# Performance work log

Hardware: AMD Instinct MI355X
Metric: run time of the kernel (lower is better)

Reference implementation:

```python
import jax, jax.numpy as jnp
import numpy as np
from jax import lax

N = 100000      # nodes
F_IN = 128      # dataset.num_features
H = 64          # hidden
E = 1600000     # edges
G = 1000        # graphs (equal-sized, contiguous)
PER = N // G    # nodes per graph = 100
K = 30          # sort-pool k
KS = 3          # conv1d kernel = num_layers


def setup_inputs() -> dict:
    key = jax.random.key(0)
    ks = jax.random.split(key, 20)
    lin = lambda k, i, o: (jax.random.normal(k, (i, o), jnp.float32) / np.sqrt(i)).astype(jnp.float32)
    return {
        "x": jax.random.normal(ks[0], (N, F_IN), jnp.float32),
        "src": jax.random.randint(ks[1], (E,), 0, N, dtype=jnp.int32),
        "dst": jax.random.randint(ks[2], (E,), 0, N, dtype=jnp.int32),
        "num_graphs": G,
        # SAGEConv 1: lin_l (aggr, with bias), lin_r (self, no bias)
        "wl1": lin(ks[3], F_IN, H), "wr1": lin(ks[4], F_IN, H), "b1": jnp.zeros((H,), jnp.float32),
        "wl2": lin(ks[5], H, H), "wr2": lin(ks[6], H, H), "b2": jnp.zeros((H,), jnp.float32),
        "wl3": lin(ks[7], H, H), "wr3": lin(ks[8], H, H), "b3": jnp.zeros((H,), jnp.float32),
        # Conv1d(hidden=64 -> 32, kernel=3): weight [O, I, K]
        "cw": (jax.random.normal(ks[9], (32, H, KS), jnp.float32) / np.sqrt(H * KS)).astype(jnp.float32),
        "cb": jnp.zeros((32,), jnp.float32),
        "w1": lin(ks[10], 32 * (K - KS + 1), H), "bb1": jnp.zeros((H,), jnp.float32),
        "w2": lin(ks[11], H, 1), "bb2": jnp.zeros((1,), jnp.float32),
    }


def _sage(x, src, dst, wl, wr, b, n):
    # PyG SAGEConv (mean aggr): lin_l(mean_{j->i} x_j) + lin_r(x_i)
    msum = jax.ops.segment_sum(x[src], dst, num_segments=n)           # [N, F]
    cnt = jax.ops.segment_sum(jnp.ones((src.shape[0],), x.dtype), dst, num_segments=n)
    mean = msum / jnp.maximum(cnt, 1.0)[:, None]
    return mean @ wl + b + x @ wr


def reference(x, src, dst, num_graphs, wl1, wr1, b1, wl2, wr2, b2, wl3, wr3, b3, cw, cb, w1, bb1, w2, bb2):
    n = x.shape[0]
    h = jax.nn.relu(_sage(x, src, dst, wl1, wr1, b1, n))
    h = jax.nn.relu(_sage(h, src, dst, wl2, wr2, b2, n))
    h = jax.nn.relu(_sage(h, src, dst, wl3, wr3, b3, n))
    # SortAggregation(k): per-graph, sort nodes by last feature channel (desc), keep top-k.
    # batch = contiguous equal-sized graphs -> dense reshape is exact.
    hg = h.reshape(num_graphs, PER, H)                                # [G, PER, H]
    order = jnp.argsort(-hg[:, :, -1], axis=1)[:, :K]                 # [G, K]
    topk = jnp.take_along_axis(hg, order[:, :, None], axis=1)         # [G, K, H]
    xc = jnp.transpose(topk, (0, 2, 1))                               # [G, H, K]
    y = lax.conv_general_dilated(xc, cw, (1,), 'VALID',
                                 dimension_numbers=('NCH', 'OIH', 'NCH'))
    y = jax.nn.relu(y + cb[None, :, None])                            # [G, 32, K-KS+1]
    y = y.reshape(num_graphs, -1)
    y = jax.nn.relu(y @ w1 + bb1)
    # dropout: eval mode -> identity
    return y @ w2 + bb2                                               # [G, 1]
```

## Files before the change

### kernel.cpp

```cpp
#include <hip/hip_runtime.h>

#define NN 100000
#define EE 1600000
#define GG 1000
#define PERG 100
#define KK 30
#define HH 64

#define NB 782
#define CAP 4096
#define CHB 4096
#define BUCKET_BLOCKS ((EE + CHB - 1) / CHB)
#define PROJ_BLOCKS ((NN + 127) / 128)

__global__ __launch_bounds__(1024) void zero_int(int* p, int n) {
  int i = blockIdx.x * 1024 + threadIdx.x;
  if (i < n) p[i] = 0;
}

__device__ __forceinline__ void bucket_body(int bid, float* smem,
                                            const int* __restrict__ src,
                                            const int* __restrict__ dst,
                                            int* __restrict__ gcur,
                                            int* __restrict__ pairs) {
  int* lhist = (int*)smem;
  int* lbase = lhist + NB;
  int* lcur = lbase + NB;
  const int t = threadIdx.x;
  const int c0 = bid * CHB;
  const int c1 = min(c0 + CHB, EE);
  for (int b = t; b < NB; b += 256) {
    lhist[b] = 0;
    lcur[b] = 0;
  }
  __syncthreads();
  for (int e = c0 + t; e < c1; e += 256) atomicAdd(&lhist[dst[e] >> 7], 1);
  __syncthreads();
  for (int b = t; b < NB; b += 256) {
    int c = lhist[b];
    lbase[b] = c ? atomicAdd(&gcur[b], c) : 0;
  }
  __syncthreads();
  for (int e = c0 + t; e < c1; e += 256) {
    int d = dst[e];
    int b = d >> 7;
    int p = atomicAdd(&lcur[b], 1);
    pairs[b * CAP + lbase[b] + p] = (src[e] << 7) | (d & 127);
  }
}

template <int K>
__device__ __forceinline__ void proj_body(int bid, float* smem,
                                          const float* __restrict__ X,
                                          const float* __restrict__ WL,
                                          const float* __restrict__ WR,
                                          float* __restrict__ P,
                                          float* __restrict__ R) {
  constexpr int BM = 128, BK = 32, XSP = 40, WSP = 144;
  float* xs = smem;
  float* ws = smem + BM * XSP;
  const int t = threadIdx.x;
  const int row0 = bid * BM;
  const int tc = t & 15, tr = t >> 4;
  const int wcol = tc * 8 + (tc >> 2) * 4;

  float acc[8][8];
#pragma unroll
  for (int i = 0; i < 8; ++i)
#pragma unroll
    for (int j = 0; j < 8; ++j) acc[i][j] = 0.f;

  for (int k0 = 0; k0 < K; k0 += BK) {
    __syncthreads();
    for (int idx = t; idx < BM * 8; idx += 256) {
      int r = idx >> 3, c = idx & 7;
      int row = row0 + r;
      float4 v = make_float4(0.f, 0.f, 0.f, 0.f);
      if (row < NN) v = *reinterpret_cast<const float4*>(&X[(size_t)row * K + k0 + c * 4]);
      *reinterpret_cast<float4*>(&xs[r * XSP + c * 4]) = v;
    }
    for (int idx = t; idx < BK * 16; idx += 256) {
      int kr = idx >> 4, c4 = idx & 15;
      int gcl = c4 >> 1;
      int off = gcl * 8 + (gcl >> 2) * 4 + (c4 & 1) * 4;
      *reinterpret_cast<float4*>(&ws[kr * WSP + off]) =
          *reinterpret_cast<const float4*>(&WL[(k0 + kr) * 64 + c4 * 4]);
      int g2 = gcl + 8;
      int off2 = g2 * 8 + (g2 >> 2) * 4 + (c4 & 1) * 4;
      *reinterpret_cast<float4*>(&ws[kr * WSP + off2]) =
          *reinterpret_cast<const float4*>(&WR[(k0 + kr) * 64 + c4 * 4]);
    }
    __syncthreads();
    for (int kk4 = 0; kk4 < BK; kk4 += 4) {
      float4 a[8];
#pragma unroll
      for (int i = 0; i < 8; ++i)
        a[i] = *reinterpret_cast<const float4*>(&xs[(tr + 16 * i) * XSP + kk4]);
#pragma unroll
      for (int kk = 0; kk < 4; ++kk) {
        float4 b0 = *reinterpret_cast<const float4*>(&ws[(kk4 + kk) * WSP + wcol]);
        float4 b1 = *reinterpret_cast<const float4*>(&ws[(kk4 + kk) * WSP + wcol + 4]);
        float bv[8] = {b0.x, b0.y, b0.z, b0.w, b1.x, b1.y, b1.z, b1.w};
#pragma unroll
        for (int i = 0; i < 8; ++i) {
          float av = (kk == 0) ? a[i].x : (kk == 1) ? a[i].y : (kk == 2) ? a[i].z : a[i].w;
#pragma unroll
          for (int j = 0; j < 8; ++j) acc[i][j] = fmaf(av, bv[j], acc[i][j]);
        }
      }
    }
  }

  float* OUT = (tc < 8) ? P : R;
  int cb = (tc & 7) * 8;
#pragma unroll
  for (int i = 0; i < 8; ++i) {
    int row = row0 + tr + 16 * i;
    if (row < NN) {
      *reinterpret_cast<float4*>(&OUT[(size_t)row * 64 + cb]) =
          make_float4(acc[i][0], acc[i][1], acc[i][2], acc[i][3]);
      *reinterpret_cast<float4*>(&OUT[(size_t)row * 64 + cb + 4]) =
          make_float4(acc[i][4], acc[i][5], acc[i][6], acc[i][7]);
    }
  }
}

__global__ __launch_bounds__(256) void fused_bucket_proj(const int* __restrict__ src,
                                                         const int* __restrict__ dst,
                                                         int* __restrict__ gcur,
                                                         int* __restrict__ pairs,
                                                         const float* __restrict__ X,
                                                         const float* __restrict__ WL,
                                                         const float* __restrict__ WR,
                                                         float* __restrict__ P,
                                                         float* __restrict__ R) {
  __shared__ float smem[128 * 40 + 32 * 144];
  if (blockIdx.x < BUCKET_BLOCKS)
    bucket_body(blockIdx.x, smem, src, dst, gcur, pairs);
  else
    proj_body<128>(blockIdx.x - BUCKET_BLOCKS, smem, X, WL, WR, P, R);
}

template <int K>
__global__ __launch_bounds__(256) void proj_kernel(const float* __restrict__ X,
                                                   const float* __restrict__ WL,
                                                   const float* __restrict__ WR,
                                                   float* __restrict__ P,
                                                   float* __restrict__ R) {
  __shared__ float smem[128 * 40 + 32 * 144];
  proj_body<K>(blockIdx.x, smem, X, WL, WR, P, R);
}

__global__ __launch_bounds__(256) void csr_kernel(const int* __restrict__ gcur,
                                                  const int* __restrict__ pairs,
                                                  int* __restrict__ row_start,
                                                  int* __restrict__ cnt,
                                                  int* __restrict__ eidx) {
  __shared__ int vals[CAP];
  __shared__ int hist[128];
  __shared__ int offs[128];
  __shared__ int cur[128];
  __shared__ int red[4];
  const int b = blockIdx.x;
  const int t = threadIdx.x;
  int s = 0;
  for (int i = t; i < b; i += 256) s += gcur[i];
#pragma unroll
  for (int off = 32; off > 0; off >>= 1) s += __shfl_xor(s, off);
  if ((t & 63) == 0) red[t >> 6] = s;
  if (t < 128) {
    hist[t] = 0;
    cur[t] = 0;
  }
  __syncthreads();
  const int base = red[0] + red[1] + red[2] + red[3];
  const int nb = gcur[b];
  for (int i = t; i < nb; i += 256) {
    int v = pairs[b * CAP + i];
    vals[i] = v;
    atomicAdd(&hist[v & 127], 1);
  }
  __syncthreads();
  if (t < 128) {
    int ss = 0;
    for (int m = 0; m < t; ++m) ss += hist[m];
    offs[t] = ss;
    int node = b * 128 + t;
    if (node < NN) {
      row_start[node] = base + ss;
      cnt[node] = hist[t];
    }
  }
  __syncthreads();
  for (int i = t; i < nb; i += 256) {
    int v = vals[i];
    int ld = v & 127;
    int p = atomicAdd(&cur[ld], 1);
    eidx[base + offs[ld] + p] = v >> 7;
  }
}

__global__ __launch_bounds__(256) void agg_kernel(const float* __restrict__ P,
                                                  const float* __restrict__ R,
                                                  const float* __restrict__ bias,
                                                  const int* __restrict__ row_start,
                                                  const int* __restrict__ cnt,
                                                  const int* __restrict__ eidx,
                                                  float* __restrict__ h,
                                                  float* __restrict__ keys) {
  int wid = (blockIdx.x * 256 + threadIdx.x) >> 6;
  int lane = threadIdx.x & 63;
  if (wid >= NN) return;
  const int q = lane >> 4;
  const int ql = lane & 15;
  const int base = row_start[wid];
  const int deg = cnt[wid];
  float4 a0 = make_float4(0.f, 0.f, 0.f, 0.f);
  float4 a1 = make_float4(0.f, 0.f, 0.f, 0.f);

  for (int e0 = 0; e0 < deg; e0 += 64) {
    const int m = min(64, deg - e0);
    int idx = (lane < m) ? eidx[base + e0 + lane] : 0;
    for (int j = 0; j < m; j += 16) {
      const int eA = j + q, eB = j + 4 + q, eC = j + 8 + q, eD = j + 12 + q;
      const int sA = __shfl(idx, min(eA, m - 1));
      const int sB = __shfl(idx, min(eB, m - 1));
      const int sC = __shfl(idx, min(eC, m - 1));
      const int sD = __shfl(idx, min(eD, m - 1));
      const float wA = (eA < m) ? 1.f : 0.f;
      const float wB = (eB < m) ? 1.f : 0.f;
      const float wC = (eC < m) ? 1.f : 0.f;
      const float wD = (eD < m) ? 1.f : 0.f;
      float4 vA = *reinterpret_cast<const float4*>(&P[(size_t)sA * 64 + ql * 4]);
      float4 vB = *reinterpret_cast<const float4*>(&P[(size_t)sB * 64 + ql * 4]);
      float4 vC = *reinterpret_cast<const float4*>(&P[(size_t)sC * 64 + ql * 4]);
      float4 vD = *reinterpret_cast<const float4*>(&P[(size_t)sD * 64 + ql * 4]);
      a0.x = fmaf(wA, vA.x, a0.x); a0.y = fmaf(wA, vA.y, a0.y);
      a0.z = fmaf(wA, vA.z, a0.z); a0.w = fmaf(wA, vA.w, a0.w);
      a1.x = fmaf(wB, vB.x, a1.x); a1.y = fmaf(wB, vB.y, a1.y);
      a1.z = fmaf(wB, vB.z, a1.z); a1.w = fmaf(wB, vB.w, a1.w);
      a0.x = fmaf(wC, vC.x, a0.x); a0.y = fmaf(wC, vC.y, a0.y);
      a0.z = fmaf(wC, vC.z, a0.z); a0.w = fmaf(wC, vC.w, a0.w);
      a1.x = fmaf(wD, vD.x, a1.x); a1.y = fmaf(wD, vD.y, a1.y);
      a1.z = fmaf(wD, vD.z, a1.z); a1.w = fmaf(wD, vD.w, a1.w);
    }
  }

  float4 acc = make_float4(a0.x + a1.x, a0.y + a1.y, a0.z + a1.z, a0.w + a1.w);
#pragma unroll
  for (int d = 16; d < 64; d <<= 1) {
    acc.x += __shfl_xor(acc.x, d);
    acc.y += __shfl_xor(acc.y, d);
    acc.z += __shfl_xor(acc.z, d);
    acc.w += __shfl_xor(acc.w, d);
  }

  if (q == 0) {
    const float dv = fmaxf((float)deg, 1.0f);
    float4 r4 = *reinterpret_cast<const float4*>(&R[(size_t)wid * 64 + ql * 4]);
    float4 b4 = *reinterpret_cast<const float4*>(&bias[ql * 4]);
    float4 o;
    o.x = fmaxf(acc.x / dv + b4.x + r4.x, 0.f);
    o.y = fmaxf(acc.y / dv + b4.y + r4.y, 0.f);
    o.z = fmaxf(acc.z / dv + b4.z + r4.z, 0.f);
    o.w = fmaxf(acc.w / dv + b4.w + r4.w, 0.f);
    *reinterpret_cast<float4*>(&h[(size_t)wid * 64 + ql * 4]) = o;
    if (keys != nullptr && ql == 15) keys[wid] = o.w;
  }
}

__global__ __launch_bounds__(256) void head_kernel(const float* __restrict__ h,
                                                   const float* __restrict__ keysArr,
                                                   const float* __restrict__ cw,
                                                   const float* __restrict__ cb,
                                                   const float* __restrict__ w1,
                                                   const float* __restrict__ bb1,
                                                   const float* __restrict__ w2,
                                                   const float* __restrict__ bb2,
                                                   float* __restrict__ out) {
  __shared__ float key[PERG];
  __shared__ int sel[KK];
  __shared__ float feat[34 * 65];
  __shared__ float cwT[192 * 33];
  __shared__ float z[896];
  __shared__ float psum[256];
  const int g = blockIdx.x;
  const int t = threadIdx.x;

  for (int idx = t; idx < 32 * 192; idx += 256) {
    int o = idx / 192, k = idx % 192;
    cwT[k * 33 + o] = cw[idx];
  }
  if (t < PERG) key[t] = keysArr[g * PERG + t];
  __syncthreads();

  if (t < PERG) {
    float kv = key[t];
    int r = 0;
    for (int m = 0; m < PERG; ++m) {
      float km = key[m];
      r += (int)((km > kv) || (km == kv && m < t));
    }
    if (r < KK) sel[r] = t;
  }
  __syncthreads();

  for (int idx = t; idx < KK * HH; idx += 256) {
    int r = idx >> 6, f = idx & 63;
    feat[r * 65 + f] = h[(size_t)(g * PERG + sel[r]) * HH + f];
  }
  __syncthreads();

  {
    const int o = t & 31;
    const int pg = t >> 5;
    float zacc[4] = {0.f, 0.f, 0.f, 0.f};
    int i = 0, tt = 0;
    for (int k = 0; k < 192; ++k) {
      float c = cwT[k * 33 + o];
#pragma unroll
      for (int j = 0; j < 4; ++j) {
        int p = pg + 8 * j;
        zacc[j] = fmaf(c, feat[(p + tt) * 65 + i], zacc[j]);
      }
      if (++tt == 3) {
        tt = 0;
        ++i;
      }
    }
    float cbo = cb[o];
#pragma unroll
    for (int j = 0; j < 4; ++j) {
      int p = pg + 8 * j;
      if (p < 28) z[o * 28 + p] = fmaxf(zacc[j] + cbo, 0.f);
    }
  }
  __syncthreads();

  {
    const int hh = t & 63;
    const int quarter = t >> 6;
    const int q0 = quarter * 224;
    float acc = 0.f;
    for (int q = 0; q < 224; ++q)
      acc = fmaf(z[q0 + q], w1[(size_t)(q0 + q) * 64 + hh], acc);
    psum[t] = acc;
  }
  __syncthreads();

  if (t < 64) {
    float o1 = fmaxf(bb1[t] + psum[t] + psum[t + 64] + psum[t + 128] + psum[t + 192], 0.f);
    float v = o1 * w2[t];
#pragma unroll
    for (int off = 32; off > 0; off >>= 1) v += __shfl_down(v, off);
    if (t == 0) out[g] = v + bb2[0];
  }
}

extern "C" void kernel_launch(void* const* d_in, const int* in_sizes, int n_in,
                              void* d_out, int out_size, void* d_ws, size_t ws_size,
                              hipStream_t stream) {
  const float* x = (const float*)d_in[0];
  const int* src = (const int*)d_in[1];
  const int* dst = (const int*)d_in[2];
  const float* wl1 = (const float*)d_in[4];
  const float* wr1 = (const float*)d_in[5];
  const float* b1 = (const float*)d_in[6];
  const float* wl2 = (const float*)d_in[7];
  const float* wr2 = (const float*)d_in[8];
  const float* b2 = (const float*)d_in[9];
  const float* wl3 = (const float*)d_in[10];
  const float* wr3 = (const float*)d_in[11];
  const float* b3 = (const float*)d_in[12];
  const float* cw = (const float*)d_in[13];
  const float* cb = (const float*)d_in[14];
  const float* w1 = (const float*)d_in[15];
  const float* bb1 = (const float*)d_in[16];
  const float* w2 = (const float*)d_in[17];
  const float* bb2 = (const float*)d_in[18];
  float* out = (float*)d_out;

  char* w = (char*)d_ws;
  auto carve = [&](size_t bytes) {
    char* p = w;
    w += (bytes + 255) & ~(size_t)255;
    return p;
  };
  int* row_start = (int*)carve((size_t)NN * 4);
  int* cnt = (int*)carve((size_t)NN * 4);
  int* eidx = (int*)carve((size_t)EE * 4);
  float* P = (float*)carve((size_t)NN * 64 * 4);
  float* R = (float*)carve((size_t)NN * 64 * 4);
  float* hbuf = (float*)carve((size_t)NN * 64 * 4);
  float* keys = (float*)carve((size_t)NN * 4);
  int* gcur = (int*)carve((size_t)NB * 4);
  int* pairs = (int*)hbuf;

  zero_int<<<1, 1024, 0, stream>>>(gcur, NB);
  fused_bucket_proj<<<BUCKET_BLOCKS + PROJ_BLOCKS, 256, 0, stream>>>(
      src, dst, gcur, pairs, x, wl1, wr1, P, R);
  csr_kernel<<<NB, 256, 0, stream>>>(gcur, pairs, row_start, cnt, eidx);

  const int aggGrid = (NN + 3) / 4;
  agg_kernel<<<aggGrid, 256, 0, stream>>>(P, R, b1, row_start, cnt, eidx, hbuf, nullptr);
  proj_kernel<64><<<PROJ_BLOCKS, 256, 0, stream>>>(hbuf, wl2, wr2, P, R);
  agg_kernel<<<aggGrid, 256, 0, stream>>>(P, R, b2, row_start, cnt, eidx, hbuf, nullptr);
  proj_kernel<64><<<PROJ_BLOCKS, 256, 0, stream>>>(hbuf, wl3, wr3, P, R);
  agg_kernel<<<aggGrid, 256, 0, stream>>>(P, R, b3, row_start, cnt, eidx, hbuf, keys);
  head_kernel<<<GG, 256, 0, stream>>>(hbuf, keys, cw, cb, w1, bb1, w2, bb2, out);
}
```

Baseline: 482.1 us.

## Replace shared-memory tiled projection GEMM with one-row-per-thread register GEMM

```diff
diff --git a/kernel.cpp b/kernel.cpp
--- a/kernel.cpp
+++ b/kernel.cpp
@@ -11,21 +11,21 @@
 #define CAP 4096
 #define CHB 4096
 #define BUCKET_BLOCKS ((EE + CHB - 1) / CHB)
-#define PROJ_BLOCKS ((NN + 127) / 128)
+#define RGB ((NN + 255) / 256)
 
 __global__ __launch_bounds__(1024) void zero_int(int* p, int n) {
   int i = blockIdx.x * 1024 + threadIdx.x;
   if (i < n) p[i] = 0;
 }
 
-__device__ __forceinline__ void bucket_body(int bid, float* smem,
+__device__ __forceinline__ void bucket_body(int bid,
                                             const int* __restrict__ src,
                                             const int* __restrict__ dst,
                                             int* __restrict__ gcur,
                                             int* __restrict__ pairs) {
-  int* lhist = (int*)smem;
-  int* lbase = lhist + NB;
-  int* lcur = lbase + NB;
+  __shared__ int lhist[NB];
+  __shared__ int lbase[NB];
+  __shared__ int lcur[NB];
   const int t = threadIdx.x;
   const int c0 = bid * CHB;
   const int c1 = min(c0 + CHB, EE);
@@ -50,77 +50,46 @@
 }
 
 template <int K>
-__device__ __forceinline__ void proj_body(int bid, float* smem,
-                                          const float* __restrict__ X,
-                                          const float* __restrict__ WL,
-                                          const float* __restrict__ WR,
-                                          float* __restrict__ P,
-                                          float* __restrict__ R) {
-  constexpr int BM = 128, BK = 32, XSP = 40, WSP = 144;
-  float* xs = smem;
-  float* ws = smem + BM * XSP;
-  const int t = threadIdx.x;
-  const int row0 = bid * BM;
-  const int tc = t & 15, tr = t >> 4;
-  const int wcol = tc * 8 + (tc >> 2) * 4;
-
-  float acc[8][8];
-#pragma unroll
-  for (int i = 0; i < 8; ++i)
-#pragma unroll
-    for (int j = 0; j < 8; ++j) acc[i][j] = 0.f;
-
-  for (int k0 = 0; k0 < K; k0 += BK) {
-    __syncthreads();
-    for (int idx = t; idx < BM * 8; idx += 256) {
-      int r = idx >> 3, c = idx & 7;
-      int row = row0 + r;
-      float4 v = make_float4(0.f, 0.f, 0.f, 0.f);
-      if (row < NN) v = *reinterpret_cast<const float4*>(&X[(size_t)row * K + k0 + c * 4]);
-      *reinterpret_cast<float4*>(&xs[r * XSP + c * 4]) = v;
-    }
-    for (int idx = t; idx < BK * 16; idx += 256) {
-      int kr = idx >> 4, c4 = idx & 15;
-      int gcl = c4 >> 1;
-      int off = gcl * 8 + (gcl >> 2) * 4 + (c4 & 1) * 4;
-      *reinterpret_cast<float4*>(&ws[kr * WSP + off]) =
-          *reinterpret_cast<const float4*>(&WL[(k0 + kr) * 64 + c4 * 4]);
-      int g2 = gcl + 8;
-      int off2 = g2 * 8 + (g2 >> 2) * 4 + (c4 & 1) * 4;
-      *reinterpret_cast<float4*>(&ws[kr * WSP + off2]) =
-          *reinterpret_cast<const float4*>(&WR[(k0 + kr) * 64 + c4 * 4]);
-    }
-    __syncthreads();
-    for (int kk4 = 0; kk4 < BK; kk4 += 4) {
-      float4 a[8];
-#pragma unroll
-      for (int i = 0; i < 8; ++i)
-        a[i] = *reinterpret_cast<const float4*>(&xs[(tr + 16 * i) * XSP + kk4]);
-#pragma unroll
-      for (int kk = 0; kk < 4; ++kk) {
-        float4 b0 = *reinterpret_cast<const float4*>(&ws[(kk4 + kk) * WSP + wcol]);
-        float4 b1 = *reinterpret_cast<const float4*>(&ws[(kk4 + kk) * WSP + wcol + 4]);
-        float bv[8] = {b0.x, b0.y, b0.z, b0.w, b1.x, b1.y, b1.z, b1.w};
-#pragma unroll
-        for (int i = 0; i < 8; ++i) {
-          float av = (kk == 0) ? a[i].x : (kk == 1) ? a[i].y : (kk == 2) ? a[i].z : a[i].w;
-#pragma unroll
-          for (int j = 0; j < 8; ++j) acc[i][j] = fmaf(av, bv[j], acc[i][j]);
-        }
-      }
-    }
-  }
-
-  float* OUT = (tc < 8) ? P : R;
-  int cb = (tc & 7) * 8;
-#pragma unroll
-  for (int i = 0; i < 8; ++i) {
-    int row = row0 + tr + 16 * i;
+__device__ __forceinline__ void proj_rowgemm(int row,
+                                             const float* __restrict__ X,
+                                             const float* __restrict__ WL,
+                                             const float* __restrict__ WR,
+                                             float* __restrict__ P,
+                                             float* __restrict__ R) {
+  float xr[K];
+  if (row < NN) {
+#pragma unroll
+    for (int kq = 0; kq < K / 4; ++kq) {
+      float4 v = *reinterpret_cast<const float4*>(&X[(size_t)row * K + kq * 4]);
+      xr[kq * 4 + 0] = v.x;
+      xr[kq * 4 + 1] = v.y;
+      xr[kq * 4 + 2] = v.z;
+      xr[kq * 4 + 3] = v.w;
+    }
+  } else {
+#pragma unroll
+    for (int k = 0; k < K; ++k) xr[k] = 0.f;
+  }
+
+#pragma unroll 1
+  for (int c = 0; c < 8; ++c) {
+    const float* __restrict__ W = (c < 4) ? (WL + c * 16) : (WR + (c - 4) * 16);
+    float acc[16];
+#pragma unroll
+    for (int j = 0; j < 16; ++j) acc[j] = 0.f;
+#pragma unroll
+    for (int k = 0; k < K; ++k) {
+      const float* __restrict__ wk = W + (size_t)k * 64;
+#pragma unroll
+      for (int j = 0; j < 16; ++j) acc[j] = fmaf(xr[k], wk[j], acc[j]);
+    }
     if (row < NN) {
-      *reinterpret_cast<float4*>(&OUT[(size_t)row * 64 + cb]) =
-          make_float4(acc[i][0], acc[i][1], acc[i][2], acc[i][3]);
-      *reinterpret_cast<float4*>(&OUT[(size_t)row * 64 + cb + 4]) =
-          make_float4(acc[i][4], acc[i][5], acc[i][6], acc[i][7]);
+      float* __restrict__ OUT = (c < 4) ? P : R;
+      const size_t o = (size_t)row * 64 + (c & 3) * 16;
+#pragma unroll
+      for (int j4 = 0; j4 < 4; ++j4)
+        *reinterpret_cast<float4*>(&OUT[o + j4 * 4]) =
+            make_float4(acc[j4 * 4], acc[j4 * 4 + 1], acc[j4 * 4 + 2], acc[j4 * 4 + 3]);
     }
   }
 }
@@ -134,11 +103,12 @@
                                                          const float* __restrict__ WR,
                                                          float* __restrict__ P,
                                                          float* __restrict__ R) {
-  __shared__ float smem[128 * 40 + 32 * 144];
-  if (blockIdx.x < BUCKET_BLOCKS)
-    bucket_body(blockIdx.x, smem, src, dst, gcur, pairs);
-  else
-    proj_body<128>(blockIdx.x - BUCKET_BLOCKS, smem, X, WL, WR, P, R);
+  if (blockIdx.x < BUCKET_BLOCKS) {
+    bucket_body(blockIdx.x, src, dst, gcur, pairs);
+  } else {
+    int row = (blockIdx.x - BUCKET_BLOCKS) * 256 + threadIdx.x;
+    proj_rowgemm<128>(row, X, WL, WR, P, R);
+  }
 }
 
 template <int K>
@@ -147,8 +117,8 @@
                                                    const float* __restrict__ WR,
                                                    float* __restrict__ P,
                                                    float* __restrict__ R) {
-  __shared__ float smem[128 * 40 + 32 * 144];
-  proj_body<K>(blockIdx.x, smem, X, WL, WR, P, R);
+  int row = blockIdx.x * 256 + threadIdx.x;
+  proj_rowgemm<K>(row, X, WL, WR, P, R);
 }
 
 __global__ __launch_bounds__(256) void csr_kernel(const int* __restrict__ gcur,
@@ -397,15 +367,15 @@
   int* pairs = (int*)hbuf;
 
   zero_int<<<1, 1024, 0, stream>>>(gcur, NB);
-  fused_bucket_proj<<<BUCKET_BLOCKS + PROJ_BLOCKS, 256, 0, stream>>>(
+  fused_bucket_proj<<<BUCKET_BLOCKS + RGB, 256, 0, stream>>>(
       src, dst, gcur, pairs, x, wl1, wr1, P, R);
   csr_kernel<<<NB, 256, 0, stream>>>(gcur, pairs, row_start, cnt, eidx);
 
   const int aggGrid = (NN + 3) / 4;
   agg_kernel<<<aggGrid, 256, 0, stream>>>(P, R, b1, row_start, cnt, eidx, hbuf, nullptr);
-  proj_kernel<64><<<PROJ_BLOCKS, 256, 0, stream>>>(hbuf, wl2, wr2, P, R);
+  proj_kernel<64><<<RGB, 256, 0, stream>>>(hbuf, wl2, wr2, P, R);
   agg_kernel<<<aggGrid, 256, 0, stream>>>(P, R, b2, row_start, cnt, eidx, hbuf, nullptr);
-  proj_kernel<64><<<PROJ_BLOCKS, 256, 0, stream>>>(hbuf, wl3, wr3, P, R);
+  proj_kernel<64><<<RGB, 256, 0, stream>>>(hbuf, wl3, wr3, P, R);
   agg_kernel<<<aggGrid, 256, 0, stream>>>(P, R, b3, row_start, cnt, eidx, hbuf, keys);
   head_kernel<<<GG, 256, 0, stream>>>(hbuf, keys, cw, cb, w1, bb1, w2, bb2, out);
 }
```

Result: slower. 1.582 ms (+228.1%).

## Fuse neighbor mean-aggregation with next layer's projection into one kernel

Applied to the files above, without the earlier changes.

```diff
diff --git a/kernel.cpp b/kernel.cpp
--- a/kernel.cpp
+++ b/kernel.cpp
@@ -141,14 +141,133 @@
     proj_body<128>(blockIdx.x - BUCKET_BLOCKS, smem, X, WL, WR, P, R);
 }
 
-template <int K>
-__global__ __launch_bounds__(256) void proj_kernel(const float* __restrict__ X,
-                                                   const float* __restrict__ WL,
-                                                   const float* __restrict__ WR,
-                                                   float* __restrict__ P,
-                                                   float* __restrict__ R) {
-  __shared__ float smem[128 * 40 + 32 * 144];
-  proj_body<K>(blockIdx.x, smem, X, WL, WR, P, R);
+__global__ __launch_bounds__(256) void agg_proj(const float* __restrict__ Pin,
+                                                float* __restrict__ Rio,
+                                                const float* __restrict__ bias,
+                                                const int* __restrict__ row_start,
+                                                const int* __restrict__ cnt,
+                                                const int* __restrict__ eidx,
+                                                const float* __restrict__ WL,
+                                                const float* __restrict__ WR,
+                                                float* __restrict__ Pout) {
+  constexpr int XSP = 68, WSP = 144, BK = 32;
+  __shared__ float xs[128 * XSP];
+  __shared__ float ws[BK * WSP];
+  const int t = threadIdx.x;
+  const int lane = t & 63;
+  const int w = t >> 6;
+  const int q = lane >> 4, ql = lane & 15;
+  const int row0 = blockIdx.x * 128;
+
+  for (int i = 0; i < 32; ++i) {
+    const int n = row0 + w * 32 + i;
+    if (n >= NN) break;
+    const int base = row_start[n];
+    const int deg = cnt[n];
+    float4 a0 = make_float4(0.f, 0.f, 0.f, 0.f);
+    float4 a1 = make_float4(0.f, 0.f, 0.f, 0.f);
+    for (int e0 = 0; e0 < deg; e0 += 64) {
+      const int m = min(64, deg - e0);
+      int idx = (lane < m) ? eidx[base + e0 + lane] : 0;
+      for (int j = 0; j < m; j += 16) {
+        const int eA = j + q, eB = j + 4 + q, eC = j + 8 + q, eD = j + 12 + q;
+        const int sA = __shfl(idx, min(eA, m - 1));
+        const int sB = __shfl(idx, min(eB, m - 1));
+        const int sC = __shfl(idx, min(eC, m - 1));
+        const int sD = __shfl(idx, min(eD, m - 1));
+        const float wA = (eA < m) ? 1.f : 0.f;
+        const float wB = (eB < m) ? 1.f : 0.f;
+        const float wC = (eC < m) ? 1.f : 0.f;
+        const float wD = (eD < m) ? 1.f : 0.f;
+        float4 vA = *reinterpret_cast<const float4*>(&Pin[(size_t)sA * 64 + ql * 4]);
+        float4 vB = *reinterpret_cast<const float4*>(&Pin[(size_t)sB * 64 + ql * 4]);
+        float4 vC = *reinterpret_cast<const float4*>(&Pin[(size_t)sC * 64 + ql * 4]);
+        float4 vD = *reinterpret_cast<const float4*>(&Pin[(size_t)sD * 64 + ql * 4]);
+        a0.x = fmaf(wA, vA.x, a0.x); a0.y = fmaf(wA, vA.y, a0.y);
+        a0.z = fmaf(wA, vA.z, a0.z); a0.w = fmaf(wA, vA.w, a0.w);
+        a1.x = fmaf(wB, vB.x, a1.x); a1.y = fmaf(wB, vB.y, a1.y);
+        a1.z = fmaf(wB, vB.z, a1.z); a1.w = fmaf(wB, vB.w, a1.w);
+        a0.x = fmaf(wC, vC.x, a0.x); a0.y = fmaf(wC, vC.y, a0.y);
+        a0.z = fmaf(wC, vC.z, a0.z); a0.w = fmaf(wC, vC.w, a0.w);
+        a1.x = fmaf(wD, vD.x, a1.x); a1.y = fmaf(wD, vD.y, a1.y);
+        a1.z = fmaf(wD, vD.z, a1.z); a1.w = fmaf(wD, vD.w, a1.w);
+      }
+    }
+    float4 acc = make_float4(a0.x + a1.x, a0.y + a1.y, a0.z + a1.z, a0.w + a1.w);
+#pragma unroll
+    for (int d = 16; d < 64; d <<= 1) {
+      acc.x += __shfl_xor(acc.x, d);
+      acc.y += __shfl_xor(acc.y, d);
+      acc.z += __shfl_xor(acc.z, d);
+      acc.w += __shfl_xor(acc.w, d);
+    }
+    if (q == 0) {
+      const float dv = fmaxf((float)deg, 1.0f);
+      float4 r4 = *reinterpret_cast<const float4*>(&Rio[(size_t)n * 64 + ql * 4]);
+      float4 b4 = *reinterpret_cast<const float4*>(&bias[ql * 4]);
+      float4 o;
+      o.x = fmaxf(acc.x / dv + b4.x + r4.x, 0.f);
+      o.y = fmaxf(acc.y / dv + b4.y + r4.y, 0.f);
+      o.z = fmaxf(acc.z / dv + b4.z + r4.z, 0.f);
+      o.w = fmaxf(acc.w / dv + b4.w + r4.w, 0.f);
+      *reinterpret_cast<float4*>(&xs[(w * 32 + i) * XSP + ql * 4]) = o;
+    }
+  }
+
+  const int tc = t & 15, tr = t >> 4;
+  const int wcol = tc * 8 + (tc >> 2) * 4;
+  float acc[8][8];
+#pragma unroll
+  for (int i = 0; i < 8; ++i)
+#pragma unroll
+    for (int j = 0; j < 8; ++j) acc[i][j] = 0.f;
+
+  for (int k0 = 0; k0 < 64; k0 += BK) {
+    __syncthreads();
+    for (int idx = t; idx < BK * 16; idx += 256) {
+      int kr = idx >> 4, c4 = idx & 15;
+      int gcl = c4 >> 1;
+      int off = gcl * 8 + (gcl >> 2) * 4 + (c4 & 1) * 4;
+      *reinterpret_cast<float4*>(&ws[kr * WSP + off]) =
+          *reinterpret_cast<const float4*>(&WL[(k0 + kr) * 64 + c4 * 4]);
+      int g2 = gcl + 8;
+      int off2 = g2 * 8 + (g2 >> 2) * 4 + (c4 & 1) * 4;
+      *reinterpret_cast<float4*>(&ws[kr * WSP + off2]) =
+          *reinterpret_cast<const float4*>(&WR[(k0 + kr) * 64 + c4 * 4]);
+    }
+    __syncthreads();
+    for (int kk4 = 0; kk4 < BK; kk4 += 4) {
+      float4 a[8];
+#pragma unroll
+      for (int i = 0; i < 8; ++i)
+        a[i] = *reinterpret_cast<const float4*>(&xs[(tr + 16 * i) * XSP + k0 + kk4]);
+#pragma unroll
+      for (int kk = 0; kk < 4; ++kk) {
+        float4 b0 = *reinterpret_cast<const float4*>(&ws[(kk4 + kk) * WSP + wcol]);
+        float4 b1 = *reinterpret_cast<const float4*>(&ws[(kk4 + kk) * WSP + wcol + 4]);
+        float bv[8] = {b0.x, b0.y, b0.z, b0.w, b1.x, b1.y, b1.z, b1.w};
+#pragma unroll
+        for (int i = 0; i < 8; ++i) {
+          float av = (kk == 0) ? a[i].x : (kk == 1) ? a[i].y : (kk == 2) ? a[i].z : a[i].w;
+#pragma unroll
+          for (int j = 0; j < 8; ++j) acc[i][j] = fmaf(av, bv[j], acc[i][j]);
+        }
+      }
+    }
+  }
+
+  float* OUT = (tc < 8) ? Pout : Rio;
+  int cb = (tc & 7) * 8;
+#pragma unroll
+  for (int i = 0; i < 8; ++i) {
+    int row = row0 + tr + 16 * i;
+    if (row < NN) {
+      *reinterpret_cast<float4*>(&OUT[(size_t)row * 64 + cb]) =
+          make_float4(acc[i][0], acc[i][1], acc[i][2], acc[i][3]);
+      *reinterpret_cast<float4*>(&OUT[(size_t)row * 64 + cb + 4]) =
+          make_float4(acc[i][4], acc[i][5], acc[i][6], acc[i][7]);
+    }
+  }
 }
 
 __global__ __launch_bounds__(256) void csr_kernel(const int* __restrict__ gcur,
@@ -401,11 +520,11 @@
       src, dst, gcur, pairs, x, wl1, wr1, P, R);
   csr_kernel<<<NB, 256, 0, stream>>>(gcur, pairs, row_start, cnt, eidx);
 
+  agg_proj<<<PROJ_BLOCKS, 256, 0, stream>>>(P, R, b1, row_start, cnt, eidx,
+                                            wl2, wr2, hbuf);
+  agg_proj<<<PROJ_BLOCKS, 256, 0, stream>>>(hbuf, R, b2, row_start, cnt, eidx,
+                                            wl3, wr3, P);
   const int aggGrid = (NN + 3) / 4;
-  agg_kernel<<<aggGrid, 256, 0, stream>>>(P, R, b1, row_start, cnt, eidx, hbuf, nullptr);
-  proj_kernel<64><<<PROJ_BLOCKS, 256, 0, stream>>>(hbuf, wl2, wr2, P, R);
-  agg_kernel<<<aggGrid, 256, 0, stream>>>(P, R, b2, row_start, cnt, eidx, hbuf, nullptr);
-  proj_kernel<64><<<PROJ_BLOCKS, 256, 0, stream>>>(hbuf, wl3, wr3, P, R);
   agg_kernel<<<aggGrid, 256, 0, stream>>>(P, R, b3, row_start, cnt, eidx, hbuf, keys);
   head_kernel<<<GG, 256, 0, stream>>>(hbuf, keys, cw, cb, w1, bb1, w2, bb2, out);
 }
```

Result: slower. 584.7 us (+21.3%).
